# Performance work log

Measured on AMD Instinct MI355X. Metric: run time of the kernel, lower is better.

Reference implementation:

```python
import jax, jax.numpy as jnp
import numpy as np

B, S, HID = 2, 2048, 2048
H = 16
Q_LORA, KV_LORA = 1536, 512
D_NOPE, D_ROPE, D_V = 128, 64, 128
D_QK = D_NOPE + D_ROPE  # 192
EPS = 1e-6


def rms_norm(x, w):
    var = jnp.mean(jnp.square(x), axis=-1, keepdims=True)
    return x * jax.lax.rsqrt(var + EPS) * w


def apply_rope(x, cos, sin):
    # x: [..., d] with interleaved (real, imag) pairs; cos/sin broadcastable to [..., d//2]
    xr = x[..., 0::2]
    xi = x[..., 1::2]
    or_ = xr * cos - xi * sin
    oi_ = xr * sin + xi * cos
    return jnp.stack([or_, oi_], axis=-1).reshape(x.shape)


def setup_inputs() -> dict:
    key = jax.random.key(0)
    ks = jax.random.split(key, 8)
    std = 0.02
    x = jax.random.normal(ks[0], (B, S, HID), dtype=jnp.float32)
    # rotary frequencies (real cos/sin pair per complex freq)
    inv_freq = 1.0 / (10000.0 ** (np.arange(0, D_ROPE, 2, dtype=np.float32) / D_ROPE))
    t = np.arange(S, dtype=np.float32)
    ang = np.outer(t, inv_freq)  # [S, D_ROPE//2]
    freqs_cis = jnp.asarray(np.stack([np.cos(ang), np.sin(ang)], axis=-1))  # [S, 32, 2]
    return {
        "x": x,
        "freqs_cis": freqs_cis,
        "wq_a": std * jax.random.normal(ks[1], (Q_LORA, HID), dtype=jnp.float32),
        "q_a_norm_w": jnp.ones((Q_LORA,), dtype=jnp.float32),
        "wq_b": std * jax.random.normal(ks[2], (H * D_QK, Q_LORA), dtype=jnp.float32),
        "wkv_a": std * jax.random.normal(ks[3], (KV_LORA + D_ROPE, HID), dtype=jnp.float32),
        "kv_norm_w": jnp.ones((KV_LORA,), dtype=jnp.float32),
        "wkv_b": std * jax.random.normal(ks[4], (H * (D_NOPE + D_V), KV_LORA), dtype=jnp.float32),
        "wo": std * jax.random.normal(ks[5], (HID, H * D_V), dtype=jnp.float32),
    }


def mla_forward(x, freqs_cis, wq_a, q_a_norm_w, wq_b, wkv_a, kv_norm_w, wkv_b, wo):
    cos = freqs_cis[..., 0]  # [S, D_ROPE//2]
    sin = freqs_cis[..., 1]
    # --- queries: low-rank down, RMSNorm, up ---
    q = rms_norm(x @ wq_a.T, q_a_norm_w) @ wq_b.T          # [B,S,H*D_QK]
    q = q.reshape(B, S, H, D_QK)
    q_nope, q_pe = q[..., :D_NOPE], q[..., D_NOPE:]
    q_pe = apply_rope(q_pe, cos[None, :, None, :], sin[None, :, None, :])
    q = jnp.concatenate([q_nope, q_pe], axis=-1)           # [B,S,H,D_QK]
    # --- kv latent + shared rope key ---
    kv_all = x @ wkv_a.T                                   # [B,S,KV_LORA+D_ROPE]
    kv_lat, k_pe = kv_all[..., :KV_LORA], kv_all[..., KV_LORA:]
    k_pe = apply_rope(k_pe, cos[None, :, :], sin[None, :, :])   # [B,S,D_ROPE]
    kv = rms_norm(kv_lat, kv_norm_w) @ wkv_b.T             # [B,S,H*(D_NOPE+D_V)]
    kv = kv.reshape(B, S, H, D_NOPE + D_V)
    k_nope, v = kv[..., :D_NOPE], kv[..., D_NOPE:]
    k = jnp.concatenate(
        [k_nope, jnp.broadcast_to(k_pe[:, :, None, :], (B, S, H, D_ROPE))], axis=-1
    )                                                      # [B,S,H,D_QK]
    # --- causal softmax attention ---
    scale = D_QK ** -0.5
    scores = jnp.einsum("bqhd,bkhd->bhqk", q, k) * scale   # [B,H,S,S]
    causal = jnp.tril(jnp.ones((S, S), dtype=bool))
    scores = jnp.where(causal, scores, jnp.finfo(scores.dtype).min)
    probs = jax.nn.softmax(scores, axis=-1)
    out = jnp.einsum("bhqk,bkhd->bqhd", probs, v)          # [B,S,H,D_V]
    return out.reshape(B, S, H * D_V) @ wo.T               # [B,S,HID]


def reference(x, freqs_cis, wq_a, q_a_norm_w, wq_b, wkv_a, kv_norm_w, wkv_b, wo):
    return mla_forward(x, freqs_cis, wq_a, q_a_norm_w, wq_b, wkv_a, kv_norm_w, wkv_b, wo)
```

## Files before the change

### kernel.cpp

```cpp
#include <hip/hip_runtime.h>

typedef __bf16 bf16_t;
typedef bf16_t bf16x8 __attribute__((ext_vector_type(8)));
typedef bf16_t bf16x4v __attribute__((ext_vector_type(4)));
typedef float f32x4 __attribute__((ext_vector_type(4)));

static constexpr float QSCALE = 0.07216878364870323f * 1.44269504088896341f;

#define AS1 __attribute__((address_space(1)))
#define AS3 __attribute__((address_space(3)))
__device__ __forceinline__ void g2lds16(const void* g, void* l) {
  __builtin_amdgcn_global_load_lds((const AS1 void*)g, (AS3 void*)l, 16, 0, 0);
}

__global__ void k_cast_bf16(const float* __restrict__ in, bf16_t* __restrict__ out, int n8) {
  int i = blockIdx.x * 256 + threadIdx.x;
  if (i >= n8) return;
  const float4* p = (const float4*)in + (size_t)i * 2;
  float4 a = p[0], b = p[1];
  bf16x8 o = {(bf16_t)a.x, (bf16_t)a.y, (bf16_t)a.z, (bf16_t)a.w,
              (bf16_t)b.x, (bf16_t)b.y, (bf16_t)b.z, (bf16_t)b.w};
  ((bf16x8*)out)[i] = o;
}

template <int MODE>
__global__ __launch_bounds__(256) void k_gemm_t(
    const bf16_t* __restrict__ A, const bf16_t* __restrict__ Bt,
    void* __restrict__ Cout, int M, int N, int K, const float* __restrict__ freqs) {
  __shared__ __align__(16) bf16_t As[128][32];
  __shared__ __align__(16) bf16_t Bs[128][32];
  const int tid = threadIdx.x;
  const int lane = tid & 63, wid = tid >> 6;
  const int wr = wid >> 1, wc = wid & 1;
  const int lr = lane & 15, lk = lane >> 4;
  const int bm = blockIdx.y * 128, bn = blockIdx.x * 128;
  f32x4 acc[4][4] = {};
  const int srow = wid * 16 + (lane >> 2);
  const int scol = (lane & 3) * 8;
  const bf16_t* a0 = A + (size_t)(bm + srow) * K + scol;
  const bf16_t* a1 = A + (size_t)(bm + 64 + srow) * K + scol;
  const bf16_t* b0 = Bt + (size_t)(bn + srow) * K + scol;
  const bf16_t* b1 = Bt + (size_t)(bn + 64 + srow) * K + scol;
  bf16_t* lA0 = &As[wid * 16][0];
  bf16_t* lA1 = &As[64 + wid * 16][0];
  bf16_t* lB0 = &Bs[wid * 16][0];
  bf16_t* lB1 = &Bs[64 + wid * 16][0];
  for (int kt = 0; kt < K; kt += 32) {
    g2lds16(a0 + kt, lA0);
    g2lds16(a1 + kt, lA1);
    g2lds16(b0 + kt, lB0);
    g2lds16(b1 + kt, lB1);
    __syncthreads();
    bf16x8 af[4], bff[4];
#pragma unroll
    for (int i = 0; i < 4; i++)
      af[i] = *(const bf16x8*)(&As[wr * 64 + i * 16 + lr][lk * 8]);
#pragma unroll
    for (int j = 0; j < 4; j++)
      bff[j] = *(const bf16x8*)(&Bs[wc * 64 + j * 16 + lr][lk * 8]);
#pragma unroll
    for (int i = 0; i < 4; i++)
#pragma unroll
      for (int j = 0; j < 4; j++)
        acc[i][j] = __builtin_amdgcn_mfma_f32_16x16x32_bf16(af[i], bff[j], acc[i][j], 0, 0, 0);
    __syncthreads();
  }
  const int crow = bm + wr * 64 + lk * 4;
  const int ccol = bn + wc * 64 + lr;
#pragma unroll
  for (int i = 0; i < 4; i++)
#pragma unroll
    for (int j = 0; j < 4; j++) {
      int col = ccol + j * 16;
      if (col < N) {
        if constexpr (MODE == 0) {
          float* C = (float*)Cout;
#pragma unroll
          for (int r = 0; r < 4; r++)
            C[(size_t)(crow + i * 16 + r) * N + col] = acc[i][j][r];
        } else if constexpr (MODE == 1) {
          bf16_t* C = (bf16_t*)Cout;
#pragma unroll
          for (int r = 0; r < 4; r++)
            C[(size_t)(crow + i * 16 + r) * N + col] = (bf16_t)acc[i][j][r];
        } else {
          bf16_t* Qd = (bf16_t*)Cout;
          int hcol = col / 192;
          int dmod = col - hcol * 192;
#pragma unroll
          for (int r = 0; r < 4; r++) {
            int row = crow + i * 16 + r;
            int bb = row >> 11, s = row & 2047;
            float v = acc[i][j][r];
            float partner = __shfl_xor(v, 1);
            if (dmod >= 128) {
              int p = (dmod - 128) >> 1;
              int pbase = ((lr & 1) == 0) ? (dmod - 128) : (dmod - 129);
              p = pbase >> 1;
              float c = freqs[s * 64 + 2 * p];
              float sn = freqs[s * 64 + 2 * p + 1];
              v = ((lr & 1) == 0) ? (v * c - partner * sn) : (partner * sn + v * c);
            }
            Qd[((size_t)(bb * 16 + hcol) * 2048 + s) * 192 + dmod] = (bf16_t)(v * QSCALE);
          }
        }
      }
    }
}

__global__ __launch_bounds__(256) void k_rms_q(const bf16_t* __restrict__ in,
                                               const float* __restrict__ w,
                                               bf16_t* __restrict__ out) {
  int row = blockIdx.x, tid = threadIdx.x;
  const bf16x8* x8 = (const bf16x8*)(in + (size_t)row * 1536);
  float ss = 0.f;
  bf16x8 v = {};
  if (tid < 192) {
    v = x8[tid];
#pragma unroll
    for (int j = 0; j < 8; j++) { float f = (float)v[j]; ss += f * f; }
  }
  for (int m = 32; m; m >>= 1) ss += __shfl_xor(ss, m);
  __shared__ float parts[4];
  if ((tid & 63) == 0) parts[tid >> 6] = ss;
  __syncthreads();
  float inv = rsqrtf((parts[0] + parts[1] + parts[2] + parts[3]) * (1.f / 1536.f) + 1e-6f);
  if (tid < 192) {
    const float4* w4 = (const float4*)(w + tid * 8);
    float4 w0 = w4[0], w1 = w4[1];
    bf16x8 o = {(bf16_t)((float)v[0] * inv * w0.x), (bf16_t)((float)v[1] * inv * w0.y),
                (bf16_t)((float)v[2] * inv * w0.z), (bf16_t)((float)v[3] * inv * w0.w),
                (bf16_t)((float)v[4] * inv * w1.x), (bf16_t)((float)v[5] * inv * w1.y),
                (bf16_t)((float)v[6] * inv * w1.z), (bf16_t)((float)v[7] * inv * w1.w)};
    *(bf16x8*)(out + (size_t)row * 1536 + tid * 8) = o;
  }
}

__global__ __launch_bounds__(256) void k_kv_norm_rope(const bf16_t* __restrict__ kvall,
                                                      const float* __restrict__ w,
                                                      const float* __restrict__ freqs,
                                                      bf16_t* __restrict__ kvn,
                                                      bf16_t* __restrict__ Kf) {
  int row = blockIdx.x, tid = threadIdx.x;
  int b = row >> 11, s = row & 2047;
  const bf16_t* x = kvall + (size_t)row * 576;
  float ss = 0.f;
  float vf[4] = {0.f, 0.f, 0.f, 0.f};
  if (tid < 128) {
    bf16x4v v4 = *(const bf16x4v*)(x + tid * 4);
#pragma unroll
    for (int j = 0; j < 4; j++) { vf[j] = (float)v4[j]; ss += vf[j] * vf[j]; }
  }
  for (int m = 32; m; m >>= 1) ss += __shfl_xor(ss, m);
  __shared__ float parts[4];
  if ((tid & 63) == 0) parts[tid >> 6] = ss;
  __syncthreads();
  float inv = rsqrtf((parts[0] + parts[1] + parts[2] + parts[3]) * (1.f / 512.f) + 1e-6f);
  if (tid < 128) {
    float4 ww = ((const float4*)w)[tid];
    bf16x4v o = {(bf16_t)(vf[0] * inv * ww.x), (bf16_t)(vf[1] * inv * ww.y),
                 (bf16_t)(vf[2] * inv * ww.z), (bf16_t)(vf[3] * inv * ww.w)};
    *(bf16x4v*)(kvn + (size_t)row * 512 + tid * 4) = o;
  }
  if (tid < 32) {
    float xr = (float)x[512 + 2 * tid], xi = (float)x[513 + 2 * tid];
    float c = freqs[s * 64 + 2 * tid], sn = freqs[s * 64 + 2 * tid + 1];
    bf16_t o0 = (bf16_t)(xr * c - xi * sn);
    bf16_t o1 = (bf16_t)(xr * sn + xi * c);
#pragma unroll
    for (int h = 0; h < 16; h++) {
      size_t base = ((size_t)(b * 16 + h) * 2048 + s) * 192 + 128 + 2 * tid;
      Kf[base] = o0;
      Kf[base + 1] = o1;
    }
  }
}

__global__ __launch_bounds__(256) void k_split_kv(const bf16_t* __restrict__ kvfull,
                                                  bf16_t* __restrict__ Kf,
                                                  bf16_t* __restrict__ Vt) {
  __shared__ bf16_t vt_l[128][66];
  int s0 = blockIdx.x * 64;
  int h = blockIdx.y;
#pragma unroll 4
  for (int i = 0; i < 32; i++) {
    int idx = i * 256 + threadIdx.x;
    int r = idx >> 7, d = idx & 127;
    int row = s0 + r;
    int b = row >> 11, s = row & 2047;
    const bf16_t* src = kvfull + (size_t)row * 4096 + h * 256;
    Kf[((size_t)(b * 16 + h) * 2048 + s) * 192 + d] = src[d];
    vt_l[d][r] = src[128 + d];
  }
  __syncthreads();
#pragma unroll 4
  for (int i = 0; i < 32; i++) {
    int idx = i * 256 + threadIdx.x;
    int d = idx >> 6, ss = idx & 63;
    int row = s0 + ss;
    int b = row >> 11, s = row & 2047;
    Vt[((size_t)(b * 16 + h) * 128 + d) * 2048 + s] = vt_l[d][ss];
  }
}

__global__ __launch_bounds__(512) void k_attn(const bf16_t* __restrict__ Q,
                                              const bf16_t* __restrict__ Kf,
                                              const bf16_t* __restrict__ Vt,
                                              bf16_t* __restrict__ O) {
  __shared__ __align__(16) bf16_t Ks[3][64][64];
  __shared__ __align__(16) bf16_t Vs[128][64];
  __shared__ __align__(16) bf16_t P[8][16][72];
  const int tid = threadIdx.x;
  const int lane = tid & 63, wid = tid >> 6;
  const int lr = lane & 15, lk = lane >> 4;
  const int qt = (int)gridDim.x - 1 - (int)blockIdx.x;
  const int qb = qt * 128;
  const int qbw = qb + wid * 16;
  const int bh = blockIdx.y;
  const int b = bh >> 4, h = bh & 15;
  const bf16_t* Qp = Q + (size_t)bh * 2048 * 192;
  const bf16_t* Kb = Kf + (size_t)bh * 2048 * 192;
  const bf16_t* Vb = Vt + (size_t)bh * 128 * 2048;
  bf16x8 bq[6];
#pragma unroll
  for (int f = 0; f < 6; f++)
    bq[f] = *(const bf16x8*)(Qp + (size_t)(qbw + lr) * 192 + f * 32 + lk * 8);
  f32x4 acc[8] = {};
  float m_s = -1e30f, l_s = 0.f;
  const int q_mine = qbw + lr;
  const int krow = tid >> 3;
  const int kc8 = tid & 7;
  const int vd1 = 64 + krow;
  bf16x8 kr0, kr1, kr2, vr0, vr1;
  auto issue = [&](int k0) {
    const bf16_t* kp = Kb + (size_t)(k0 + krow) * 192 + kc8 * 8;
    kr0 = *(const bf16x8*)(kp);
    kr1 = *(const bf16x8*)(kp + 64);
    kr2 = *(const bf16x8*)(kp + 128);
    vr0 = *(const bf16x8*)(Vb + (size_t)krow * 2048 + k0 + kc8 * 8);
    vr1 = *(const bf16x8*)(Vb + (size_t)vd1 * 2048 + k0 + kc8 * 8);
  };
  auto commit = [&]() {
    *(bf16x8*)(&Ks[0][krow][((kc8 + krow) & 7) * 8]) = kr0;
    *(bf16x8*)(&Ks[1][krow][((kc8 + krow) & 7) * 8]) = kr1;
    *(bf16x8*)(&Ks[2][krow][((kc8 + krow) & 7) * 8]) = kr2;
    *(bf16x8*)(&Vs[krow][((kc8 + krow) & 7) * 8]) = vr0;
    *(bf16x8*)(&Vs[vd1][((kc8 + vd1) & 7) * 8]) = vr1;
  };
  const int nkt = qt * 2 + 2;
  issue(0);
  commit();
  __syncthreads();
  for (int kt = 0; kt < nkt; kt++) {
    const int k0 = kt * 64;
    if (kt + 1 < nkt) issue(k0 + 64);
    if (k0 <= qbw + 15) {
      f32x4 sc[4];
#pragma unroll
      for (int hh = 0; hh < 4; hh++) {
        f32x4 a = {};
        const int row = hh * 16 + lr;
#pragma unroll
        for (int f = 0; f < 6; f++) {
          const int cc = (f & 1) * 4 + lk;
          bf16x8 ak = *(const bf16x8*)(&Ks[f >> 1][row][((cc + row) & 7) * 8]);
          a = __builtin_amdgcn_mfma_f32_16x16x32_bf16(ak, bq[f], a, 0, 0, 0);
        }
        sc[hh] = a;
      }
      if (k0 + 63 > qbw) {
#pragma unroll
        for (int hh = 0; hh < 4; hh++) {
          int key = k0 + hh * 16 + lk * 4;
#pragma unroll
          for (int r = 0; r < 4; r++)
            if (key + r > q_mine) sc[hh][r] = -1e30f;
        }
      }
      float t0 = fmaxf(fmaxf(sc[0][0], sc[0][1]), fmaxf(sc[0][2], sc[0][3]));
      float t1 = fmaxf(fmaxf(sc[1][0], sc[1][1]), fmaxf(sc[1][2], sc[1][3]));
      float t2 = fmaxf(fmaxf(sc[2][0], sc[2][1]), fmaxf(sc[2][2], sc[2][3]));
      float t3 = fmaxf(fmaxf(sc[3][0], sc[3][1]), fmaxf(sc[3][2], sc[3][3]));
      float tmax = fmaxf(fmaxf(t0, t1), fmaxf(t2, t3));
      tmax = fmaxf(tmax, __shfl_xor(tmax, 16));
      tmax = fmaxf(tmax, __shfl_xor(tmax, 32));
      float mn = fmaxf(m_s, tmax);
      float alpha = exp2f(m_s - mn);
      m_s = mn;
      float sm = 0.f;
#pragma unroll
      for (int hh = 0; hh < 4; hh++) {
#pragma unroll
        for (int r = 0; r < 4; r++) {
          float p = exp2f(sc[hh][r] - mn);
          sc[hh][r] = p;
          sm += p;
        }
      }
      sm += __shfl_xor(sm, 16);
      sm += __shfl_xor(sm, 32);
      l_s = l_s * alpha + sm;
#pragma unroll
      for (int hh = 0; hh < 4; hh++) {
        int c8 = hh * 2 + (lk >> 1);
        int coff = ((c8 + lr) & 7) * 8 + (lk & 1) * 4;
        bf16x4v pv = {(bf16_t)sc[hh][0], (bf16_t)sc[hh][1], (bf16_t)sc[hh][2], (bf16_t)sc[hh][3]};
        *(bf16x4v*)(&P[wid][lr][coff]) = pv;
      }
      float ab[4];
#pragma unroll
      for (int r = 0; r < 4; r++) ab[r] = __shfl(alpha, lk * 4 + r);
#pragma unroll
      for (int j = 0; j < 8; j++)
#pragma unroll
        for (int r = 0; r < 4; r++) acc[j][r] *= ab[r];
#pragma unroll
      for (int s2 = 0; s2 < 2; s2++) {
        bf16x8 pa = *(const bf16x8*)(&P[wid][lr][((s2 * 4 + lk + lr) & 7) * 8]);
#pragma unroll
        for (int j = 0; j < 8; j++) {
          const int d = j * 16 + lr;
          bf16x8 bv = *(const bf16x8*)(&Vs[d][((s2 * 4 + lk + d) & 7) * 8]);
          acc[j] = __builtin_amdgcn_mfma_f32_16x16x32_bf16(pa, bv, acc[j], 0, 0, 0);
        }
      }
    }
    __syncthreads();
    if (kt + 1 < nkt) {
      commit();
      __syncthreads();
    }
  }
  float linv = 1.f / l_s;
  float lb[4];
#pragma unroll
  for (int r = 0; r < 4; r++) lb[r] = __shfl(linv, lk * 4 + r);
  size_t orow = (size_t)b * 2048 + qbw + lk * 4;
#pragma unroll
  for (int j = 0; j < 8; j++)
#pragma unroll
    for (int r = 0; r < 4; r++)
      O[(orow + r) * 2048 + h * 128 + j * 16 + lr] = (bf16_t)(acc[j][r] * lb[r]);
}

extern "C" void kernel_launch(void* const* d_in, const int* in_sizes, int n_in,
                              void* d_out, int out_size, void* d_ws, size_t ws_size,
                              hipStream_t stream) {
  const float* x = (const float*)d_in[0];
  const float* freqs = (const float*)d_in[1];
  const float* wq_a = (const float*)d_in[2];
  const float* q_norm_w = (const float*)d_in[3];
  const float* wq_b = (const float*)d_in[4];
  const float* wkv_a = (const float*)d_in[5];
  const float* kv_norm_w = (const float*)d_in[6];
  const float* wkv_b = (const float*)d_in[7];
  const float* wo = (const float*)d_in[8];
  float* out = (float*)d_out;
  char* ws = (char*)d_ws;

  bf16_t* kvallb = (bf16_t*)(ws);
  bf16_t* kvfullb = (bf16_t*)(ws + 8388608);
  bf16_t* qab = (bf16_t*)(ws + 50331648);
  bf16_t* xbf = (bf16_t*)(ws + 67108864);
  bf16_t* wqab = (bf16_t*)(ws + 83886080);
  bf16_t* wqbb = (bf16_t*)(ws + 90177536);
  bf16_t* wkvab = (bf16_t*)(ws + 99614720);
  bf16_t* wkvbb = (bf16_t*)(ws + 101974016);
  bf16_t* wob = (bf16_t*)(ws + 106168320);
  bf16_t* qan = (bf16_t*)(ws + 114556928);
  bf16_t* kvn = (bf16_t*)(ws + 127139840);
  bf16_t* Qb = (bf16_t*)(ws + 131334144);
  bf16_t* Kb = (bf16_t*)(ws + 156499968);
  bf16_t* Vtb = (bf16_t*)(ws + 181665792);
  bf16_t* aob = (bf16_t*)(ws + 198443008);
  (void)in_sizes; (void)n_in; (void)out_size; (void)ws_size;

  auto cast = [&](const float* src, bf16_t* dst, int n) {
    int n8 = n / 8;
    k_cast_bf16<<<(n8 + 255) / 256, 256, 0, stream>>>(src, dst, n8);
  };
  cast(x, xbf, 8388608);
  cast(wq_a, wqab, 3145728);
  cast(wq_b, wqbb, 4718592);
  cast(wkv_a, wkvab, 1179648);
  cast(wkv_b, wkvbb, 2097152);
  cast(wo, wob, 4194304);

  k_gemm_t<1><<<dim3(5, 32), 256, 0, stream>>>(xbf, wkvab, kvallb, 4096, 576, 2048, nullptr);
  k_kv_norm_rope<<<4096, 256, 0, stream>>>(kvallb, kv_norm_w, freqs, kvn, Kb);
  k_gemm_t<1><<<dim3(32, 32), 256, 0, stream>>>(kvn, wkvbb, kvfullb, 4096, 4096, 512, nullptr);
  k_split_kv<<<dim3(64, 16), 256, 0, stream>>>(kvfullb, Kb, Vtb);
  k_gemm_t<1><<<dim3(12, 32), 256, 0, stream>>>(xbf, wqab, qab, 4096, 1536, 2048, nullptr);
  k_rms_q<<<4096, 256, 0, stream>>>(qab, q_norm_w, qan);
  k_gemm_t<2><<<dim3(24, 32), 256, 0, stream>>>(qan, wqbb, Qb, 4096, 3072, 1536, freqs);
  k_attn<<<dim3(16, 32), 512, 0, stream>>>(Qb, Kb, Vtb, aob);
  k_gemm_t<0><<<dim3(16, 32), 256, 0, stream>>>(aob, wob, out, 4096, 2048, 2048, nullptr);
}
```

Before: 579.8 us.

## Fuse casts and q/kv down-projections, write K directly, double-buffer attention with async LDS loads

The six cast launches become one kernel. The q_a and kv_a down-projections merge into a single GEMM by placing the wkv_a weights right after wq_a, giving N=2112. The kv up-projection GEMM now writes K_nope straight into the K layout and V into a compact buffer, so the split kernel only transposes V. The attention kernel switches to double-buffered K/V tiles loaded with global_load_lds and XOR swizzling, which removes the register staging and the second barrier per iteration. The risk is whether the contiguous weight placement and the new swizzle indexing stay correct.

```diff
diff --git a/kernel.cpp b/kernel.cpp
--- a/kernel.cpp
+++ b/kernel.cpp
@@ -13,20 +13,34 @@
   __builtin_amdgcn_global_load_lds((const AS1 void*)g, (AS3 void*)l, 16, 0, 0);
 }
 
-__global__ void k_cast_bf16(const float* __restrict__ in, bf16_t* __restrict__ out, int n8) {
-  int i = blockIdx.x * 256 + threadIdx.x;
-  if (i >= n8) return;
-  const float4* p = (const float4*)in + (size_t)i * 2;
+__global__ __launch_bounds__(256) void k_cast_all(
+    const float* __restrict__ s0, const float* __restrict__ s1, const float* __restrict__ s2,
+    const float* __restrict__ s3, const float* __restrict__ s4, const float* __restrict__ s5,
+    bf16_t* __restrict__ d0, bf16_t* __restrict__ d1, bf16_t* __restrict__ d2,
+    bf16_t* __restrict__ d3, bf16_t* __restrict__ d4, bf16_t* __restrict__ d5,
+    int c1, int c2, int c3, int c4, int c5, int c6) {
+  int g = blockIdx.x * 256 + threadIdx.x;
+  const float* s; bf16_t* d; int off;
+  if (g < c1) { s = s0; d = d0; off = 0; }
+  else if (g < c2) { s = s1; d = d1; off = c1; }
+  else if (g < c3) { s = s2; d = d2; off = c2; }
+  else if (g < c4) { s = s3; d = d3; off = c3; }
+  else if (g < c5) { s = s4; d = d4; off = c4; }
+  else if (g < c6) { s = s5; d = d5; off = c5; }
+  else return;
+  int i = g - off;
+  const float4* p = (const float4*)s + (size_t)i * 2;
   float4 a = p[0], b = p[1];
   bf16x8 o = {(bf16_t)a.x, (bf16_t)a.y, (bf16_t)a.z, (bf16_t)a.w,
               (bf16_t)b.x, (bf16_t)b.y, (bf16_t)b.z, (bf16_t)b.w};
-  ((bf16x8*)out)[i] = o;
+  ((bf16x8*)d)[i] = o;
 }
 
 template <int MODE>
 __global__ __launch_bounds__(256) void k_gemm_t(
     const bf16_t* __restrict__ A, const bf16_t* __restrict__ Bt,
-    void* __restrict__ Cout, int M, int N, int K, const float* __restrict__ freqs) {
+    void* __restrict__ Cout, int M, int N, int K, const float* __restrict__ freqs,
+    bf16_t* __restrict__ aux) {
   __shared__ __align__(16) bf16_t As[128][32];
   __shared__ __align__(16) bf16_t Bs[128][32];
   const int tid = threadIdx.x;
@@ -83,7 +97,7 @@
 #pragma unroll
           for (int r = 0; r < 4; r++)
             C[(size_t)(crow + i * 16 + r) * N + col] = (bf16_t)acc[i][j][r];
-        } else {
+        } else if constexpr (MODE == 2) {
           bf16_t* Qd = (bf16_t*)Cout;
           int hcol = col / 192;
           int dmod = col - hcol * 192;
@@ -94,15 +108,30 @@
             float v = acc[i][j][r];
             float partner = __shfl_xor(v, 1);
             if (dmod >= 128) {
-              int p = (dmod - 128) >> 1;
               int pbase = ((lr & 1) == 0) ? (dmod - 128) : (dmod - 129);
-              p = pbase >> 1;
+              int p = pbase >> 1;
               float c = freqs[s * 64 + 2 * p];
               float sn = freqs[s * 64 + 2 * p + 1];
               v = ((lr & 1) == 0) ? (v * c - partner * sn) : (partner * sn + v * c);
             }
             Qd[((size_t)(bb * 16 + hcol) * 2048 + s) * 192 + dmod] = (bf16_t)(v * QSCALE);
           }
+        } else {
+          int h = bn >> 8;
+          int d = col & 127;
+          if ((bn & 128) == 0) {
+#pragma unroll
+            for (int r = 0; r < 4; r++) {
+              int row = crow + i * 16 + r;
+              int bb = row >> 11, s = row & 2047;
+              aux[((size_t)(bb * 16 + h) * 2048 + s) * 192 + d] = (bf16_t)acc[i][j][r];
+            }
+          } else {
+            bf16_t* C = (bf16_t*)Cout;
+#pragma unroll
+            for (int r = 0; r < 4; r++)
+              C[(size_t)(crow + i * 16 + r) * 2048 + h * 128 + d] = (bf16_t)acc[i][j][r];
+          }
         }
       }
     }
@@ -112,7 +141,7 @@
                                                const float* __restrict__ w,
                                                bf16_t* __restrict__ out) {
   int row = blockIdx.x, tid = threadIdx.x;
-  const bf16x8* x8 = (const bf16x8*)(in + (size_t)row * 1536);
+  const bf16x8* x8 = (const bf16x8*)(in + (size_t)row * 2112);
   float ss = 0.f;
   bf16x8 v = {};
   if (tid < 192) {
@@ -136,14 +165,14 @@
   }
 }
 
-__global__ __launch_bounds__(256) void k_kv_norm_rope(const bf16_t* __restrict__ kvall,
+__global__ __launch_bounds__(256) void k_kv_norm_rope(const bf16_t* __restrict__ qkva,
                                                       const float* __restrict__ w,
                                                       const float* __restrict__ freqs,
                                                       bf16_t* __restrict__ kvn,
                                                       bf16_t* __restrict__ Kf) {
   int row = blockIdx.x, tid = threadIdx.x;
   int b = row >> 11, s = row & 2047;
-  const bf16_t* x = kvall + (size_t)row * 576;
+  const bf16_t* x = qkva + (size_t)row * 2112 + 1536;
   float ss = 0.f;
   float vf[4] = {0.f, 0.f, 0.f, 0.f};
   if (tid < 128) {
@@ -176,9 +205,8 @@
   }
 }
 
-__global__ __launch_bounds__(256) void k_split_kv(const bf16_t* __restrict__ kvfull,
-                                                  bf16_t* __restrict__ Kf,
-                                                  bf16_t* __restrict__ Vt) {
+__global__ __launch_bounds__(256) void k_split_v(const bf16_t* __restrict__ Vc,
+                                                 bf16_t* __restrict__ Vt) {
   __shared__ bf16_t vt_l[128][66];
   int s0 = blockIdx.x * 64;
   int h = blockIdx.y;
@@ -186,11 +214,7 @@
   for (int i = 0; i < 32; i++) {
     int idx = i * 256 + threadIdx.x;
     int r = idx >> 7, d = idx & 127;
-    int row = s0 + r;
-    int b = row >> 11, s = row & 2047;
-    const bf16_t* src = kvfull + (size_t)row * 4096 + h * 256;
-    Kf[((size_t)(b * 16 + h) * 2048 + s) * 192 + d] = src[d];
-    vt_l[d][r] = src[128 + d];
+    vt_l[d][r] = Vc[(size_t)(s0 + r) * 2048 + h * 128 + d];
   }
   __syncthreads();
 #pragma unroll 4
@@ -207,12 +231,13 @@
                                               const bf16_t* __restrict__ Kf,
                                               const bf16_t* __restrict__ Vt,
                                               bf16_t* __restrict__ O) {
-  __shared__ __align__(16) bf16_t Ks[3][64][64];
-  __shared__ __align__(16) bf16_t Vs[128][64];
-  __shared__ __align__(16) bf16_t P[8][16][72];
+  __shared__ __align__(16) bf16_t Ks[2][3][64][64];
+  __shared__ __align__(16) bf16_t Vs[2][128][64];
+  __shared__ __align__(16) bf16_t P[8][16][64];
   const int tid = threadIdx.x;
   const int lane = tid & 63, wid = tid >> 6;
   const int lr = lane & 15, lk = lane >> 4;
+  const int r8 = lane >> 3, c8 = lane & 7;
   const int qt = (int)gridDim.x - 1 - (int)blockIdx.x;
   const int qb = qt * 128;
   const int qbw = qb + wid * 16;
@@ -228,32 +253,29 @@
   f32x4 acc[8] = {};
   float m_s = -1e30f, l_s = 0.f;
   const int q_mine = qbw + lr;
-  const int krow = tid >> 3;
-  const int kc8 = tid & 7;
-  const int vd1 = 64 + krow;
-  bf16x8 kr0, kr1, kr2, vr0, vr1;
-  auto issue = [&](int k0) {
-    const bf16_t* kp = Kb + (size_t)(k0 + krow) * 192 + kc8 * 8;
-    kr0 = *(const bf16x8*)(kp);
-    kr1 = *(const bf16x8*)(kp + 64);
-    kr2 = *(const bf16x8*)(kp + 128);
-    vr0 = *(const bf16x8*)(Vb + (size_t)krow * 2048 + k0 + kc8 * 8);
-    vr1 = *(const bf16x8*)(Vb + (size_t)vd1 * 2048 + k0 + kc8 * 8);
-  };
-  auto commit = [&]() {
-    *(bf16x8*)(&Ks[0][krow][((kc8 + krow) & 7) * 8]) = kr0;
-    *(bf16x8*)(&Ks[1][krow][((kc8 + krow) & 7) * 8]) = kr1;
-    *(bf16x8*)(&Ks[2][krow][((kc8 + krow) & 7) * 8]) = kr2;
-    *(bf16x8*)(&Vs[krow][((kc8 + krow) & 7) * 8]) = vr0;
-    *(bf16x8*)(&Vs[vd1][((kc8 + vd1) & 7) * 8]) = vr1;
+  auto stage = [&](int buf, int k0) {
+#pragma unroll
+    for (int t = 0; t < 3; t++) {
+      int i = wid * 3 + t;
+      int p = i >> 3, rb = i & 7;
+      int row = rb * 8 + r8;
+      g2lds16(Kb + (size_t)(k0 + row) * 192 + p * 64 + ((c8 ^ (row & 7)) * 8),
+              &Ks[buf][p][row][c8 * 8]);
+    }
+#pragma unroll
+    for (int t = 0; t < 2; t++) {
+      int i = wid * 2 + t;
+      int d = i * 8 + r8;
+      g2lds16(Vb + (size_t)d * 2048 + k0 + ((c8 ^ (d & 7)) * 8), &Vs[buf][d][c8 * 8]);
+    }
   };
   const int nkt = qt * 2 + 2;
-  issue(0);
-  commit();
+  stage(0, 0);
   __syncthreads();
+  int buf = 0;
   for (int kt = 0; kt < nkt; kt++) {
     const int k0 = kt * 64;
-    if (kt + 1 < nkt) issue(k0 + 64);
+    if (kt + 1 < nkt) stage(buf ^ 1, k0 + 64);
     if (k0 <= qbw + 15) {
       f32x4 sc[4];
 #pragma unroll
@@ -263,7 +285,7 @@
 #pragma unroll
         for (int f = 0; f < 6; f++) {
           const int cc = (f & 1) * 4 + lk;
-          bf16x8 ak = *(const bf16x8*)(&Ks[f >> 1][row][((cc + row) & 7) * 8]);
+          bf16x8 ak = *(const bf16x8*)(&Ks[buf][f >> 1][row][((cc ^ (row & 7)) & 7) * 8]);
           a = __builtin_amdgcn_mfma_f32_16x16x32_bf16(ak, bq[f], a, 0, 0, 0);
         }
         sc[hh] = a;
@@ -302,8 +324,8 @@
       l_s = l_s * alpha + sm;
 #pragma unroll
       for (int hh = 0; hh < 4; hh++) {
-        int c8 = hh * 2 + (lk >> 1);
-        int coff = ((c8 + lr) & 7) * 8 + (lk & 1) * 4;
+        int c = hh * 2 + (lk >> 1);
+        int coff = ((c ^ (lr & 7)) * 8) + (lk & 1) * 4;
         bf16x4v pv = {(bf16_t)sc[hh][0], (bf16_t)sc[hh][1], (bf16_t)sc[hh][2], (bf16_t)sc[hh][3]};
         *(bf16x4v*)(&P[wid][lr][coff]) = pv;
       }
@@ -316,20 +338,17 @@
         for (int r = 0; r < 4; r++) acc[j][r] *= ab[r];
 #pragma unroll
       for (int s2 = 0; s2 < 2; s2++) {
-        bf16x8 pa = *(const bf16x8*)(&P[wid][lr][((s2 * 4 + lk + lr) & 7) * 8]);
+        bf16x8 pa = *(const bf16x8*)(&P[wid][lr][((s2 * 4 + lk) ^ (lr & 7)) * 8]);
 #pragma unroll
         for (int j = 0; j < 8; j++) {
           const int d = j * 16 + lr;
-          bf16x8 bv = *(const bf16x8*)(&Vs[d][((s2 * 4 + lk + d) & 7) * 8]);
+          bf16x8 bv = *(const bf16x8*)(&Vs[buf][d][((s2 * 4 + lk) ^ (d & 7)) * 8]);
           acc[j] = __builtin_amdgcn_mfma_f32_16x16x32_bf16(pa, bv, acc[j], 0, 0, 0);
         }
       }
     }
     __syncthreads();
-    if (kt + 1 < nkt) {
-      commit();
-      __syncthreads();
-    }
+    buf ^= 1;
   }
   float linv = 1.f / l_s;
   float lb[4];
@@ -358,13 +377,12 @@
   float* out = (float*)d_out;
   char* ws = (char*)d_ws;
 
-  bf16_t* kvallb = (bf16_t*)(ws);
-  bf16_t* kvfullb = (bf16_t*)(ws + 8388608);
-  bf16_t* qab = (bf16_t*)(ws + 50331648);
+  bf16_t* qkvab = (bf16_t*)(ws);
+  bf16_t* Vc = (bf16_t*)(ws + 25165824);
   bf16_t* xbf = (bf16_t*)(ws + 67108864);
   bf16_t* wqab = (bf16_t*)(ws + 83886080);
-  bf16_t* wqbb = (bf16_t*)(ws + 90177536);
-  bf16_t* wkvab = (bf16_t*)(ws + 99614720);
+  bf16_t* wkvab = (bf16_t*)(ws + 90177536);
+  bf16_t* wqbb = (bf16_t*)(ws + 92536832);
   bf16_t* wkvbb = (bf16_t*)(ws + 101974016);
   bf16_t* wob = (bf16_t*)(ws + 106168320);
   bf16_t* qan = (bf16_t*)(ws + 114556928);
@@ -375,24 +393,21 @@
   bf16_t* aob = (bf16_t*)(ws + 198443008);
   (void)in_sizes; (void)n_in; (void)out_size; (void)ws_size;
 
-  auto cast = [&](const float* src, bf16_t* dst, int n) {
-    int n8 = n / 8;
-    k_cast_bf16<<<(n8 + 255) / 256, 256, 0, stream>>>(src, dst, n8);
-  };
-  cast(x, xbf, 8388608);
-  cast(wq_a, wqab, 3145728);
-  cast(wq_b, wqbb, 4718592);
-  cast(wkv_a, wkvab, 1179648);
-  cast(wkv_b, wkvbb, 2097152);
-  cast(wo, wob, 4194304);
-
-  k_gemm_t<1><<<dim3(5, 32), 256, 0, stream>>>(xbf, wkvab, kvallb, 4096, 576, 2048, nullptr);
-  k_kv_norm_rope<<<4096, 256, 0, stream>>>(kvallb, kv_norm_w, freqs, kvn, Kb);
-  k_gemm_t<1><<<dim3(32, 32), 256, 0, stream>>>(kvn, wkvbb, kvfullb, 4096, 4096, 512, nullptr);
-  k_split_kv<<<dim3(64, 16), 256, 0, stream>>>(kvfullb, Kb, Vtb);
-  k_gemm_t<1><<<dim3(12, 32), 256, 0, stream>>>(xbf, wqab, qab, 4096, 1536, 2048, nullptr);
-  k_rms_q<<<4096, 256, 0, stream>>>(qab, q_norm_w, qan);
-  k_gemm_t<2><<<dim3(24, 32), 256, 0, stream>>>(qan, wqbb, Qb, 4096, 3072, 1536, freqs);
+  {
+    int n_x = 1048576, n_qa = 393216, n_kva = 147456, n_qb = 589824, n_kvb = 262144, n_o = 524288;
+    int c1 = n_x, c2 = c1 + n_qa, c3 = c2 + n_kva, c4 = c3 + n_qb, c5 = c4 + n_kvb, c6 = c5 + n_o;
+    k_cast_all<<<(c6 + 255) / 256, 256, 0, stream>>>(
+        x, wq_a, wkv_a, wq_b, wkv_b, wo,
+        xbf, wqab, wkvab, wqbb, wkvbb, wob,
+        c1, c2, c3, c4, c5, c6);
+  }
+
+  k_gemm_t<1><<<dim3(17, 32), 256, 0, stream>>>(xbf, wqab, qkvab, 4096, 2112, 2048, nullptr, nullptr);
+  k_kv_norm_rope<<<4096, 256, 0, stream>>>(qkvab, kv_norm_w, freqs, kvn, Kb);
+  k_gemm_t<3><<<dim3(32, 32), 256, 0, stream>>>(kvn, wkvbb, Vc, 4096, 4096, 512, nullptr, Kb);
+  k_split_v<<<dim3(64, 16), 256, 0, stream>>>(Vc, Vtb);
+  k_rms_q<<<4096, 256, 0, stream>>>(qkvab, q_norm_w, qan);
+  k_gemm_t<2><<<dim3(24, 32), 256, 0, stream>>>(qan, wqbb, Qb, 4096, 3072, 1536, freqs, nullptr);
   k_attn<<<dim3(16, 32), 512, 0, stream>>>(Qb, Kb, Vtb, aob);
-  k_gemm_t<0><<<dim3(16, 32), 256, 0, stream>>>(aob, wob, out, 4096, 2048, 2048, nullptr);
-}
+  k_gemm_t<0><<<dim3(16, 32), 256, 0, stream>>>(aob, wob, out, 4096, 2048, 2048, nullptr, nullptr);
+}
```

Result: faster. 527.9 us (-9.0%).
